# Kernel optimization log

Hardware: AMD Instinct MI355X
Metric: run time of the kernel (lower is better)

The kernel has to match this reference:

```python
import jax, jax.numpy as jnp
import numpy as np

IMG = 128; P = 16; ND = IMG // P; N = ND * ND  # 64 patches
INF = 3 * P * P      # 768 flattened patch features
ATT = 768; HID = 3072; OUT = 768; B = 64
EPS = 1e-5


def setup_inputs() -> dict:
    key = jax.random.key(0)
    ks = jax.random.split(key, 24)
    w = lambda k, shape: jax.random.normal(k, shape, jnp.float32) * 0.02
    return {
        "x": jax.random.normal(ks[0], (B, 3, IMG, IMG), jnp.float32),
        # per-patch q/k/v projections: [n, in, out] weights, [n, out] biases
        "Wq": w(ks[1], (N, INF, ATT)), "bq": w(ks[2], (N, ATT)),
        "Wk": w(ks[3], (N, INF, ATT)), "bk": w(ks[4], (N, ATT)),
        "Wv": w(ks[5], (N, INF, ATT)), "bv": w(ks[6], (N, ATT)),
        "ln_g": jnp.ones((ATT,), jnp.float32), "ln_b": jnp.zeros((ATT,), jnp.float32),
        "p1_w": w(ks[7], (INF, ATT)), "p1_b": w(ks[8], (ATT,)),
        "w0": w(ks[9], (ATT, HID)),  "b0": w(ks[10], (HID,)),
        "w1": w(ks[11], (HID, HID)), "b1": w(ks[12], (HID,)),
        "w2": w(ks[13], (HID, HID)), "b2": w(ks[14], (HID,)),
        "w3": w(ks[15], (HID, HID)), "b3": w(ks[16], (HID,)),
        "w4": w(ks[17], (HID, OUT)), "b4": w(ks[18], (OUT,)),
        "p2_w": w(ks[19], (ATT, OUT)), "p2_b": w(ks[20], (OUT,)),
    }


def _forward(x, Wq, bq, Wk, bk, Wv, bv, ln_g, ln_b, p1_w, p1_b,
             w0, b0, w1, b1, w2, b2, w3, b3, w4, b4, p2_w, p2_b):
    b_ = x.shape[0]
    # patch split (row-major over (i,j) blocks) then flatten channel*patch dims
    flat = x.reshape(b_, 3, ND, P, ND, P).transpose(0, 2, 4, 1, 3, 5).reshape(b_, N, INF)
    # per-patch projections, attention taken ACROSS the batch dim (as in source)
    q = jnp.einsum('bnf,nfd->bnd', flat, Wq) + bq
    k = jnp.einsum('bnf,nfd->bnd', flat, Wk) + bk
    v = jnp.einsum('bnf,nfd->bnd', flat, Wv) + bv
    scores = jnp.einsum('bnd,cnd->nbc', q, k) / jnp.sqrt(jnp.float32(ATT))  # [n,B,B]
    attn = jnp.einsum('nbc,cnd->bnd', jax.nn.softmax(scores, axis=-1), v)  # [B,n,ATT]
    # LayerNorm(att_features)
    mu = attn.mean(-1, keepdims=True)
    var = ((attn - mu) ** 2).mean(-1, keepdims=True)
    ln = (attn - mu) / jnp.sqrt(var + EPS) * ln_g + ln_b
    att = ln + flat @ p1_w + p1_b
    # linear stack (no nonlinearity in the source)
    h = att @ w0 + b0
    h = h @ w1 + b1
    h = h @ w2 + b2
    h = h @ w3 + b3
    h = h @ w4 + b4
    proj = h + att @ p2_w + p2_b
    return jax.nn.softmax(proj, axis=2)


def reference(x, Wq, bq, Wk, bk, Wv, bv, ln_g, ln_b, p1_w, p1_b,
              w0, b0, w1, b1, w2, b2, w3, b3, w4, b4, p2_w, p2_b):
    return _forward(x, Wq, bq, Wk, bk, Wv, bv, ln_g, ln_b, p1_w, p1_b,
                    w0, b0, w1, b1, w2, b2, w3, b3, w4, b4, p2_w, p2_b)
```

## Files before the change

### kernel.cpp

```cpp
#include <hip/hip_runtime.h>
#include <hip/hip_bf16.h>

using bf16 = __bf16;
using bf16x8 = __bf16 __attribute__((ext_vector_type(8)));
using f32x4 = float __attribute__((ext_vector_type(4)));

static constexpr long ROWEL = 64L * 768;

__device__ __forceinline__ void async16(void* lds, const void* g)
{
    __builtin_amdgcn_global_load_lds((const __attribute__((address_space(1))) void*)g,
                                     (__attribute__((address_space(3))) void*)lds, 16, 0, 0);
}

__global__ __launch_bounds__(256) void k_patchify(const float* __restrict__ x, bf16* __restrict__ flat)
{
    const int n = blockIdx.x;
    const int b = blockIdx.y;
    const int i_ = n >> 3, j_ = n & 7;
    for (int it = 0; it < 3; ++it) {
        int f = threadIdx.x + it * 256;
        int c = f >> 8, rem = f & 255, pi = rem >> 4, pj = rem & 15;
        float v = x[(((long)(b * 3 + c)) << 14) + ((i_ * 16 + pi) << 7) + (j_ * 16 + pj)];
        flat[(long)b * ROWEL + n * 768 + f] = (bf16)v;
    }
}

__global__ __launch_bounds__(256) void k_cvt_t2(
    const float* __restrict__ W0, bf16* __restrict__ T0,
    const float* __restrict__ W1, bf16* __restrict__ T1)
{
    const int z = blockIdx.z;
    const float* W = z ? W1 : W0;
    bf16* Wt = z ? T1 : T0;
    const int Kd = z ? 768 : 3072, Nd = 768;
    if (z && blockIdx.x >= 12) return;
    __shared__ bf16 T[64 * 66];
    const int k0 = blockIdx.x * 64, n0 = blockIdx.y * 64;
    const int tid = threadIdx.x;
    const int kr = tid >> 4, nc = (tid & 15) * 4;
#pragma unroll
    for (int i = 0; i < 4; ++i) {
        f32x4 v = *(const f32x4*)(W + (long)(k0 + kr + i * 16) * Nd + n0 + nc);
#pragma unroll
        for (int e = 0; e < 4; ++e)
            T[(kr + i * 16) * 66 + nc + e] = (bf16)v[e];
    }
    __syncthreads();
    const int nr = tid >> 3, ks = (tid & 7) * 8;
#pragma unroll
    for (int it = 0; it < 2; ++it) {
        int n = nr + it * 32;
        bf16x8 o;
#pragma unroll
        for (int j = 0; j < 8; ++j) o[j] = T[(ks + j) * 66 + n];
        *(bf16x8*)(Wt + (long)(n0 + n) * Kd + k0 + ks) = o;
    }
}

__global__ __launch_bounds__(256) void k_cast4(
    const float* __restrict__ s0, bf16* __restrict__ d0,
    const float* __restrict__ s1, bf16* __restrict__ d1,
    const float* __restrict__ s2, bf16* __restrict__ d2,
    const float* __restrict__ s3, bf16* __restrict__ d3)
{
    const int z = blockIdx.y;
    const float* W = z == 0 ? s0 : z == 1 ? s1 : z == 2 ? s2 : s3;
    bf16* o = z == 0 ? d0 : z == 1 ? d1 : z == 2 ? d2 : d3;
    const long nelem = z == 0 ? 768L * 3072 : 3072L * 3072;
    long i = ((long)blockIdx.x * 256 + threadIdx.x) * 8;
    if (i >= nelem) return;
    f32x4 a = *(const f32x4*)(W + i);
    f32x4 b = *(const f32x4*)(W + i + 4);
    bf16x8 v;
#pragma unroll
    for (int e = 0; e < 4; ++e) { v[e] = (bf16)a[e]; v[4 + e] = (bf16)b[e]; }
    *(bf16x8*)(o + i) = v;
}

template<int BM, int BN>
__global__ __launch_bounds__(256) void k_gemm_bt(
    const bf16* __restrict__ A, long lda,
    const bf16* __restrict__ Bt, long ldb,
    int K,
    const float* __restrict__ bias,
    const float* __restrict__ addm,
    const float* __restrict__ addt, long atld,
    bf16* __restrict__ Cb, float* __restrict__ Cf, long ldc)
{
    constexpr int WM = BM / 2, WN = BN / 2, FM = WM / 16, FN = WN / 16;
    __shared__ bf16 As[2][BM * 32];
    __shared__ bf16 Bs[2][BN * 32];
    const int tid = threadIdx.x, lane = tid & 63, wave = tid >> 6;
    const int wm = wave >> 1, wn = wave & 1;
    const long m0 = (long)blockIdx.x * BM, n0 = (long)blockIdx.y * BN;

    f32x4 acc[FM][FN];
#pragma unroll
    for (int i = 0; i < FM; ++i)
#pragma unroll
        for (int j = 0; j < FN; ++j) acc[i][j] = (f32x4){0.f, 0.f, 0.f, 0.f};

    const int nk = K >> 5;

    auto stage = [&](int buf, int kt) {
        const long kb = (long)kt * 32;
#pragma unroll
        for (int i = 0; i < BM / 64; ++i) {
            const int c = i * 256 + tid;
            const int r = c >> 2, seg = c & 3;
            async16(&As[buf][(i * 256 + wave * 64) * 8], A + (m0 + r) * lda + kb + seg * 8);
        }
#pragma unroll
        for (int i = 0; i < BN / 64; ++i) {
            const int c = i * 256 + tid;
            const int r = c >> 2, seg = c & 3;
            async16(&Bs[buf][(i * 256 + wave * 64) * 8], Bt + (n0 + r) * ldb + kb + seg * 8);
        }
    };

    stage(0, 0);
    __syncthreads();
    int cur = 0;
    for (int kt = 0; kt < nk; ++kt) {
        if (kt + 1 < nk) stage(cur ^ 1, kt + 1);
        bf16x8 af[FM], bfr[FN];
#pragma unroll
        for (int i = 0; i < FM; ++i)
            af[i] = *(const bf16x8*)&As[cur][(wm * WM + i * 16 + (lane & 15)) * 32 + (lane >> 4) * 8];
#pragma unroll
        for (int j = 0; j < FN; ++j)
            bfr[j] = *(const bf16x8*)&Bs[cur][(wn * WN + j * 16 + (lane & 15)) * 32 + (lane >> 4) * 8];
#pragma unroll
        for (int i = 0; i < FM; ++i)
#pragma unroll
            for (int j = 0; j < FN; ++j)
                acc[i][j] = __builtin_amdgcn_mfma_f32_16x16x32_bf16(af[i], bfr[j], acc[i][j], 0, 0, 0);
        __syncthreads();
        cur ^= 1;
    }

#pragma unroll
    for (int j = 0; j < FN; ++j) {
        const long col = n0 + wn * WN + j * 16 + (lane & 15);
        const float bb = bias ? bias[col] : 0.f;
#pragma unroll
        for (int i = 0; i < FM; ++i) {
#pragma unroll
            for (int r = 0; r < 4; ++r) {
                const long row = m0 + wm * WM + i * 16 + (lane >> 4) * 4 + r;
                const long idx = row * ldc + col;
                float v = acc[i][j][r] + bb;
                if (addm) v += addm[idx];
                if (addt) v += addt[col * atld + row];
                if (Cb) Cb[idx] = (bf16)v;
                if (Cf) Cf[idx] = v;
            }
        }
    }
}

__global__ __launch_bounds__(256) void k_qkv(
    const bf16* __restrict__ flat,
    const float* __restrict__ Wq, const float* __restrict__ Wk, const float* __restrict__ Wv,
    const float* __restrict__ bq, const float* __restrict__ bk, const float* __restrict__ bv,
    bf16* __restrict__ qo, bf16* __restrict__ ko, bf16* __restrict__ vo)
{
    const int zz = blockIdx.z;
    const float* W = zz == 0 ? Wq : zz == 1 ? Wk : Wv;
    const float* bias = zz == 0 ? bq : zz == 1 ? bk : bv;
    bf16* out = zz == 0 ? qo : zz == 1 ? ko : vo;

    __shared__ bf16 As[2][64 * 32];
    __shared__ float Bs[2][32 * 64];
    const int tid = threadIdx.x, lane = tid & 63, wave = tid >> 6;
    const int wm = wave >> 1, wn = wave & 1;
    const int n0 = blockIdx.x * 64;
    const int z = blockIdx.y;
    const float* Wz = W + (long)z * 589824;

    f32x4 acc[2][2];
#pragma unroll
    for (int i = 0; i < 2; ++i)
#pragma unroll
        for (int j = 0; j < 2; ++j) acc[i][j] = (f32x4){0.f, 0.f, 0.f, 0.f};

    auto stage = [&](int buf, int kt) {
        const int kb = kt * 32;
        {
            const int r = tid >> 2, seg = tid & 3;
            async16(&As[buf][wave * 512], flat + (long)r * ROWEL + z * 768 + kb + seg * 8);
        }
#pragma unroll
        for (int i = 0; i < 2; ++i) {
            const int c = i * 256 + tid;
            const int kl = c >> 4, nn = (c & 15) * 4;
            async16(&Bs[buf][(i * 256 + wave * 64) * 4], Wz + (long)(kb + kl) * 768 + n0 + nn);
        }
    };

    stage(0, 0);
    __syncthreads();
    int cur = 0;
    for (int kt = 0; kt < 24; ++kt) {
        if (kt + 1 < 24) stage(cur ^ 1, kt + 1);
        bf16x8 af[2], bfr[2];
#pragma unroll
        for (int i = 0; i < 2; ++i)
            af[i] = *(const bf16x8*)&As[cur][(wm * 32 + i * 16 + (lane & 15)) * 32 + (lane >> 4) * 8];
#pragma unroll
        for (int j = 0; j < 2; ++j) {
            const int n = wn * 32 + j * 16 + (lane & 15);
            const int kf = (lane >> 4) * 8;
            bf16x8 b;
#pragma unroll
            for (int e = 0; e < 8; ++e) b[e] = (bf16)Bs[cur][(kf + e) * 64 + n];
            bfr[j] = b;
        }
#pragma unroll
        for (int i = 0; i < 2; ++i)
#pragma unroll
            for (int j = 0; j < 2; ++j)
                acc[i][j] = __builtin_amdgcn_mfma_f32_16x16x32_bf16(af[i], bfr[j], acc[i][j], 0, 0, 0);
        __syncthreads();
        cur ^= 1;
    }

#pragma unroll
    for (int j = 0; j < 2; ++j) {
        const int col = n0 + wn * 32 + j * 16 + (lane & 15);
        const float bb = bias[z * 768 + col];
#pragma unroll
        for (int i = 0; i < 2; ++i) {
#pragma unroll
            for (int r = 0; r < 4; ++r) {
                const int row = wm * 32 + i * 16 + (lane >> 4) * 4 + r;
                out[(long)row * ROWEL + z * 768 + col] = (bf16)(acc[i][j][r] + bb);
            }
        }
    }
}

template<typename TW>
__global__ __launch_bounds__(256) void k_vm2(
    const float* __restrict__ Pin, const float* __restrict__ bin, const TW* __restrict__ W,
    int K, int N, float* __restrict__ Pout)
{
    __shared__ float red[4][64];
    const int tid = threadIdx.x;
    const int nl = tid & 63, kq = tid >> 6;
    const int n = blockIdx.x * 64 + nl;
    const int kc = blockIdx.y;
    const int kchunk = K / 8, kslice = kchunk / 4;
    const int k0 = kc * kchunk + kq * kslice;
    float acc = 0.f;
#pragma unroll 4
    for (int k = k0; k < k0 + kslice; ++k) {
        float vk = bin[k];
        if (Pin) {
#pragma unroll
            for (int j = 0; j < 8; ++j) vk += Pin[(long)j * K + k];
        }
        acc += vk * (float)W[(long)k * N + n];
    }
    red[kq][nl] = acc;
    __syncthreads();
    if (kq == 0)
        Pout[(long)kc * N + n] = red[0][nl] + red[1][nl] + red[2][nl] + red[3][nl];
}

__global__ __launch_bounds__(256) void k_vred(
    const float* __restrict__ P, const float* __restrict__ b1, const float* __restrict__ b2,
    int N, float* __restrict__ out)
{
    const int n = blockIdx.x * 256 + threadIdx.x;
    if (n >= N) return;
    float s = b1[n] + (b2 ? b2[n] : 0.f);
#pragma unroll
    for (int j = 0; j < 8; ++j) s += P[(long)j * N + n];
    out[n] = s;
}

__global__ __launch_bounds__(256) void k_attn(
    const bf16* __restrict__ q, const bf16* __restrict__ k, const bf16* __restrict__ v,
    float* __restrict__ attn)
{
    const int n = blockIdx.x;
    __shared__ bf16 QT[64 * 72];
    __shared__ bf16 KT[64 * 72];
    __shared__ float S[64 * 66];
    __shared__ bf16 P[64 * 72];
    __shared__ bf16 VT[128 * 72];

    const int tid = threadIdx.x, lane = tid & 63, wave = tid >> 6;
    const int wm = wave >> 1, wn = wave & 1;

    f32x4 accs[2][2];
#pragma unroll
    for (int i = 0; i < 2; ++i)
#pragma unroll
        for (int j = 0; j < 2; ++j) accs[i][j] = (f32x4){0.f, 0.f, 0.f, 0.f};

    for (int kt = 0; kt < 12; ++kt) {
#pragma unroll
        for (int i = 0; i < 2; ++i) {
            int cid = tid + i * 256;
            int r = cid >> 3, seg = cid & 7;
            *(bf16x8*)&QT[r * 72 + seg * 8] = *(const bf16x8*)(q + (long)r * ROWEL + n * 768 + kt * 64 + seg * 8);
            *(bf16x8*)&KT[r * 72 + seg * 8] = *(const bf16x8*)(k + (long)r * ROWEL + n * 768 + kt * 64 + seg * 8);
        }
        __syncthreads();
#pragma unroll
        for (int ks = 0; ks < 2; ++ks) {
            bf16x8 qa[2], kb[2];
#pragma unroll
            for (int i = 0; i < 2; ++i)
                qa[i] = *(const bf16x8*)&QT[(wm * 32 + i * 16 + (lane & 15)) * 72 + ks * 32 + (lane >> 4) * 8];
#pragma unroll
            for (int j = 0; j < 2; ++j)
                kb[j] = *(const bf16x8*)&KT[(wn * 32 + j * 16 + (lane & 15)) * 72 + ks * 32 + (lane >> 4) * 8];
#pragma unroll
            for (int i = 0; i < 2; ++i)
#pragma unroll
                for (int j = 0; j < 2; ++j)
                    accs[i][j] = __builtin_amdgcn_mfma_f32_16x16x32_bf16(qa[i], kb[j], accs[i][j], 0, 0, 0);
        }
        __syncthreads();
    }
    const float sc = 0.03608439182435161f;
#pragma unroll
    for (int i = 0; i < 2; ++i)
#pragma unroll
        for (int j = 0; j < 2; ++j)
#pragma unroll
            for (int r = 0; r < 4; ++r)
                S[(wm * 32 + i * 16 + (lane >> 4) * 4 + r) * 66 + wn * 32 + j * 16 + (lane & 15)] = accs[i][j][r] * sc;
    __syncthreads();

    {
        int r = tid >> 2, l4 = tid & 3;
        float m = -1e30f;
        for (int c = l4; c < 64; c += 4) m = fmaxf(m, S[r * 66 + c]);
        m = fmaxf(m, __shfl_xor(m, 1));
        m = fmaxf(m, __shfl_xor(m, 2));
        float s = 0.f;
        for (int c = l4; c < 64; c += 4) { float e = __expf(S[r * 66 + c] - m); S[r * 66 + c] = e; s += e; }
        s += __shfl_xor(s, 1);
        s += __shfl_xor(s, 2);
        float inv = 1.f / s;
        for (int c = l4; c < 64; c += 4) P[r * 72 + c] = (bf16)(S[r * 66 + c] * inv);
    }
    __syncthreads();

    for (int dc = 0; dc < 6; ++dc) {
#pragma unroll
        for (int i = 0; i < 4; ++i) {
            int cid = tid + i * 256;
            int c = cid >> 4, seg = cid & 15;
            bf16x8 vv = *(const bf16x8*)(v + (long)c * ROWEL + n * 768 + dc * 128 + seg * 8);
#pragma unroll
            for (int e = 0; e < 8; ++e)
                VT[(seg * 8 + e) * 72 + c] = vv[e];
        }
        __syncthreads();
        f32x4 acco[2][4];
#pragma unroll
        for (int i = 0; i < 2; ++i)
#pragma unroll
            for (int j = 0; j < 4; ++j) acco[i][j] = (f32x4){0.f, 0.f, 0.f, 0.f};
#pragma unroll
        for (int ks = 0; ks < 2; ++ks) {
            bf16x8 pa[2], vb[4];
#pragma unroll
            for (int i = 0; i < 2; ++i)
                pa[i] = *(const bf16x8*)&P[(wm * 32 + i * 16 + (lane & 15)) * 72 + ks * 32 + (lane >> 4) * 8];
#pragma unroll
            for (int j = 0; j < 4; ++j)
                vb[j] = *(const bf16x8*)&VT[(wn * 64 + j * 16 + (lane & 15)) * 72 + ks * 32 + (lane >> 4) * 8];
#pragma unroll
            for (int i = 0; i < 2; ++i)
#pragma unroll
                for (int j = 0; j < 4; ++j)
                    acco[i][j] = __builtin_amdgcn_mfma_f32_16x16x32_bf16(pa[i], vb[j], acco[i][j], 0, 0, 0);
        }
#pragma unroll
        for (int i = 0; i < 2; ++i)
#pragma unroll
            for (int j = 0; j < 4; ++j)
#pragma unroll
                for (int r = 0; r < 4; ++r) {
                    long b = wm * 32 + i * 16 + (lane >> 4) * 4 + r;
                    int d = dc * 128 + wn * 64 + j * 16 + (lane & 15);
                    attn[b * ROWEL + n * 768 + d] = acco[i][j][r];
                }
        __syncthreads();
    }
}

__global__ __launch_bounds__(256) void k_ln(float* __restrict__ a,
                                            const float* __restrict__ g, const float* __restrict__ bb)
{
    const long row = blockIdx.x * 4 + (threadIdx.x >> 6);
    const int lane = threadIdx.x & 63;
    float* p = a + row * 768;
    f32x4 xv[3];
    float s = 0.f;
#pragma unroll
    for (int c = 0; c < 3; ++c) {
        xv[c] = *(const f32x4*)(p + c * 256 + lane * 4);
        s += xv[c][0] + xv[c][1] + xv[c][2] + xv[c][3];
    }
#pragma unroll
    for (int o = 1; o < 64; o <<= 1) s += __shfl_xor(s, o);
    const float mu = s * (1.f / 768.f);
    float vs = 0.f;
#pragma unroll
    for (int c = 0; c < 3; ++c)
#pragma unroll
        for (int e = 0; e < 4; ++e) { float d = xv[c][e] - mu; vs += d * d; }
#pragma unroll
    for (int o = 1; o < 64; o <<= 1) vs += __shfl_xor(vs, o);
    const float rstd = rsqrtf(vs * (1.f / 768.f) + 1e-5f);
#pragma unroll
    for (int c = 0; c < 3; ++c)
#pragma unroll
        for (int e = 0; e < 4; ++e) {
            int col = c * 256 + lane * 4 + e;
            p[col] = (xv[c][e] - mu) * rstd * g[col] + bb[col];
        }
}

__global__ __launch_bounds__(256) void k_softmax(float* __restrict__ o)
{
    const long row = blockIdx.x * 4 + (threadIdx.x >> 6);
    const int lane = threadIdx.x & 63;
    float* p = o + row * 768;
    f32x4 xv[3];
    float m = -1e30f;
#pragma unroll
    for (int c = 0; c < 3; ++c) {
        xv[c] = *(const f32x4*)(p + c * 256 + lane * 4);
        m = fmaxf(m, fmaxf(fmaxf(xv[c][0], xv[c][1]), fmaxf(xv[c][2], xv[c][3])));
    }
#pragma unroll
    for (int o2 = 1; o2 < 64; o2 <<= 1) m = fmaxf(m, __shfl_xor(m, o2));
    float s = 0.f;
#pragma unroll
    for (int c = 0; c < 3; ++c)
#pragma unroll
        for (int e = 0; e < 4; ++e) { float ev = __expf(xv[c][e] - m); xv[c][e] = ev; s += ev; }
#pragma unroll
    for (int o2 = 1; o2 < 64; o2 <<= 1) s += __shfl_xor(s, o2);
    const float inv = 1.f / s;
#pragma unroll
    for (int c = 0; c < 3; ++c)
        *(f32x4*)(p + c * 256 + lane * 4) = xv[c] * inv;
}

extern "C" void kernel_launch(void* const* d_in, const int* in_sizes, int n_in,
                              void* d_out, int out_size, void* d_ws, size_t ws_size,
                              hipStream_t stream)
{
    const float* x   = (const float*)d_in[0];
    const float* Wq  = (const float*)d_in[1];
    const float* bq  = (const float*)d_in[2];
    const float* Wk  = (const float*)d_in[3];
    const float* bk  = (const float*)d_in[4];
    const float* Wv  = (const float*)d_in[5];
    const float* bv  = (const float*)d_in[6];
    const float* lng = (const float*)d_in[7];
    const float* lnb = (const float*)d_in[8];
    const float* p1w = (const float*)d_in[9];
    const float* p1b = (const float*)d_in[10];
    const float* w0  = (const float*)d_in[11];
    const float* b0  = (const float*)d_in[12];
    const float* w1  = (const float*)d_in[13];
    const float* b1  = (const float*)d_in[14];
    const float* w2  = (const float*)d_in[15];
    const float* b2  = (const float*)d_in[16];
    const float* w3  = (const float*)d_in[17];
    const float* b3  = (const float*)d_in[18];
    const float* w4  = (const float*)d_in[19];
    const float* b4  = (const float*)d_in[20];
    const float* p2w = (const float*)d_in[21];
    const float* p2b = (const float*)d_in[22];
    float* out = (float*)d_out;

    char* wsbase = (char*)d_ws;
    size_t off = 0;
    auto alloc = [&](size_t bytes) { char* p = wsbase + off; off += (bytes + 255) & ~(size_t)255; return p; };
    bf16*  flat = (bf16*)alloc(4096L * 768 * 2);
    bf16*  qb   = (bf16*)alloc(4096L * 768 * 2);
    bf16*  kb   = (bf16*)alloc(4096L * 768 * 2);
    bf16*  vb2  = (bf16*)alloc(4096L * 768 * 2);
    float* attn = (float*)alloc(4096L * 768 * 4);
    bf16*  att  = (bf16*)alloc(4096L * 768 * 2);
    bf16*  p1t  = (bf16*)alloc(768L * 768 * 2);
    bf16*  w4t  = (bf16*)alloc(768L * 3072 * 2);
    bf16*  w0c  = (bf16*)alloc(768L * 3072 * 2);
    bf16*  w1c  = (bf16*)alloc(3072L * 3072 * 2);
    bf16*  w2c  = (bf16*)alloc(3072L * 3072 * 2);
    bf16*  w3c  = (bf16*)alloc(3072L * 3072 * 2);
    bf16*  M1   = (bf16*)alloc(768L * 3072 * 2);
    bf16*  M2   = (bf16*)alloc(768L * 3072 * 2);
    bf16*  M3   = (bf16*)alloc(768L * 3072 * 2);
    bf16*  Mt   = (bf16*)alloc(768L * 768 * 2);
    float* vPa  = (float*)alloc(8L * 3072 * 4);
    float* vPb  = (float*)alloc(8L * 3072 * 4);
    float* c4   = (float*)alloc(768 * 4);
    if (off > ws_size) return;

    k_patchify<<<dim3(64, 64), 256, 0, stream>>>(x, flat);
    k_cast4<<<dim3(4608, 4), 256, 0, stream>>>(w0, w0c, w1, w1c, w2, w2c, w3, w3c);
    k_cvt_t2<<<dim3(48, 12, 2), 256, 0, stream>>>(w4, w4t, p1w, p1t);

    k_qkv<<<dim3(12, 64, 3), 256, 0, stream>>>(flat, Wq, Wk, Wv, bq, bk, bv, qb, kb, vb2);

    k_attn<<<64, 256, 0, stream>>>(qb, kb, vb2, attn);
    k_ln<<<1024, 256, 0, stream>>>(attn, lng, lnb);
    k_gemm_bt<64, 128><<<dim3(64, 6), 256, 0, stream>>>(flat, 768, p1t, 768, 768, p1b, attn, nullptr, 0, att, nullptr, 768);

    k_gemm_bt<64, 64><<<dim3(12, 48), 256, 0, stream>>>(w4t, 3072, w3c, 3072, 3072, nullptr, nullptr, nullptr, 0, M1, nullptr, 3072);
    k_gemm_bt<64, 64><<<dim3(12, 48), 256, 0, stream>>>(M1, 3072, w2c, 3072, 3072, nullptr, nullptr, nullptr, 0, M2, nullptr, 3072);
    k_gemm_bt<64, 64><<<dim3(12, 48), 256, 0, stream>>>(M2, 3072, w1c, 3072, 3072, nullptr, nullptr, nullptr, 0, M3, nullptr, 3072);
    k_gemm_bt<64, 64><<<dim3(12, 12), 256, 0, stream>>>(M3, 3072, w0c, 3072, 3072, nullptr, nullptr, p2w, 768, Mt, nullptr, 768);

    k_vm2<bf16><<<dim3(48, 8), 256, 0, stream>>>(nullptr, b0, w1c, 3072, 3072, vPa);
    k_vm2<bf16><<<dim3(48, 8), 256, 0, stream>>>(vPa, b1, w2c, 3072, 3072, vPb);
    k_vm2<bf16><<<dim3(48, 8), 256, 0, stream>>>(vPb, b2, w3c, 3072, 3072, vPa);
    k_vm2<float><<<dim3(12, 8), 256, 0, stream>>>(vPa, b3, w4, 3072, 768, vPb);
    k_vred<<<3, 256, 0, stream>>>(vPb, b4, p2b, 768, c4);

    k_gemm_bt<64, 128><<<dim3(64, 6), 256, 0, stream>>>(att, 768, Mt, 768, 768, c4, nullptr, nullptr, 0, nullptr, out, 768);
    k_softmax<<<1024, 256, 0, stream>>>(out);
}
```

Measured before the change: 606.5 us.

## Split-K the weight-chain GEMMs and use smaller tiles for activation GEMMs

```diff
diff --git a/kernel.cpp b/kernel.cpp
--- a/kernel.cpp
+++ b/kernel.cpp
@@ -2,6 +2,7 @@
 #include <hip/hip_bf16.h>
 
 using bf16 = __bf16;
+using bf16x4 = __bf16 __attribute__((ext_vector_type(4)));
 using bf16x8 = __bf16 __attribute__((ext_vector_type(8)));
 using f32x4 = float __attribute__((ext_vector_type(4)));
 
@@ -85,7 +86,6 @@
     int K,
     const float* __restrict__ bias,
     const float* __restrict__ addm,
-    const float* __restrict__ addt, long atld,
     bf16* __restrict__ Cb, float* __restrict__ Cf, long ldc)
 {
     constexpr int WM = BM / 2, WN = BN / 2, FM = WM / 16, FN = WN / 16;
@@ -152,11 +152,112 @@
                 const long idx = row * ldc + col;
                 float v = acc[i][j][r] + bb;
                 if (addm) v += addm[idx];
-                if (addt) v += addt[col * atld + row];
                 if (Cb) Cb[idx] = (bf16)v;
                 if (Cf) Cf[idx] = v;
             }
         }
+    }
+}
+
+template<int BM, int BN>
+__global__ __launch_bounds__(256) void k_gemm_btsk(
+    const bf16* __restrict__ A, long lda,
+    const bf16* __restrict__ Bt, long ldb,
+    int Ks,
+    float* __restrict__ Cp, long zstride, long ldc)
+{
+    constexpr int WM = BM / 2, WN = BN / 2, FM = WM / 16, FN = WN / 16;
+    __shared__ bf16 As[2][BM * 32];
+    __shared__ bf16 Bs[2][BN * 32];
+    const int tid = threadIdx.x, lane = tid & 63, wave = tid >> 6;
+    const int wm = wave >> 1, wn = wave & 1;
+    const long m0 = (long)blockIdx.x * BM, n0 = (long)blockIdx.y * BN;
+    const long kofs = (long)blockIdx.z * Ks;
+
+    f32x4 acc[FM][FN];
+#pragma unroll
+    for (int i = 0; i < FM; ++i)
+#pragma unroll
+        for (int j = 0; j < FN; ++j) acc[i][j] = (f32x4){0.f, 0.f, 0.f, 0.f};
+
+    const int nk = Ks >> 5;
+
+    auto stage = [&](int buf, int kt) {
+        const long kb = kofs + (long)kt * 32;
+#pragma unroll
+        for (int i = 0; i < BM / 64; ++i) {
+            const int c = i * 256 + tid;
+            const int r = c >> 2, seg = c & 3;
+            async16(&As[buf][(i * 256 + wave * 64) * 8], A + (m0 + r) * lda + kb + seg * 8);
+        }
+#pragma unroll
+        for (int i = 0; i < BN / 64; ++i) {
+            const int c = i * 256 + tid;
+            const int r = c >> 2, seg = c & 3;
+            async16(&Bs[buf][(i * 256 + wave * 64) * 8], Bt + (n0 + r) * ldb + kb + seg * 8);
+        }
+    };
+
+    stage(0, 0);
+    __syncthreads();
+    int cur = 0;
+    for (int kt = 0; kt < nk; ++kt) {
+        if (kt + 1 < nk) stage(cur ^ 1, kt + 1);
+        bf16x8 af[FM], bfr[FN];
+#pragma unroll
+        for (int i = 0; i < FM; ++i)
+            af[i] = *(const bf16x8*)&As[cur][(wm * WM + i * 16 + (lane & 15)) * 32 + (lane >> 4) * 8];
+#pragma unroll
+        for (int j = 0; j < FN; ++j)
+            bfr[j] = *(const bf16x8*)&Bs[cur][(wn * WN + j * 16 + (lane & 15)) * 32 + (lane >> 4) * 8];
+#pragma unroll
+        for (int i = 0; i < FM; ++i)
+#pragma unroll
+            for (int j = 0; j < FN; ++j)
+                acc[i][j] = __builtin_amdgcn_mfma_f32_16x16x32_bf16(af[i], bfr[j], acc[i][j], 0, 0, 0);
+        __syncthreads();
+        cur ^= 1;
+    }
+
+    float* Cz = Cp + (long)blockIdx.z * zstride;
+#pragma unroll
+    for (int j = 0; j < FN; ++j) {
+        const long col = n0 + wn * WN + j * 16 + (lane & 15);
+#pragma unroll
+        for (int i = 0; i < FM; ++i)
+#pragma unroll
+            for (int r = 0; r < 4; ++r) {
+                const long row = m0 + wm * WM + i * 16 + (lane >> 4) * 4 + r;
+                Cz[row * ldc + col] = acc[i][j][r];
+            }
+    }
+}
+
+__global__ __launch_bounds__(256) void k_skadd(
+    const float* __restrict__ P, long zstride, int S, long nelem, bf16* __restrict__ out)
+{
+    long i = ((long)blockIdx.x * 256 + threadIdx.x) * 4;
+    if (i >= nelem) return;
+    f32x4 s = *(const f32x4*)(P + i);
+    for (int z = 1; z < S; ++z) {
+        f32x4 p = *(const f32x4*)(P + (long)z * zstride + i);
+        s += p;
+    }
+    bf16x4 o;
+#pragma unroll
+    for (int e = 0; e < 4; ++e) o[e] = (bf16)s[e];
+    *(bf16x4*)(out + i) = o;
+}
+
+__global__ __launch_bounds__(256) void k_skaddT(
+    const float* __restrict__ P, long zstride, int S,
+    const float* __restrict__ p2w, bf16* __restrict__ Mt)
+{
+    const int n = blockIdx.x;
+    for (int k = threadIdx.x; k < 768; k += 256) {
+        float s = p2w[(long)k * 768 + n];
+        for (int z = 0; z < S; ++z) s += P[(long)z * zstride + n * 768 + k];
+        Mt[n * 768 + k] = (bf16)s;
     }
 }
 
@@ -505,11 +606,15 @@
     bf16*  M2   = (bf16*)alloc(768L * 3072 * 2);
     bf16*  M3   = (bf16*)alloc(768L * 3072 * 2);
     bf16*  Mt   = (bf16*)alloc(768L * 768 * 2);
+    float* Cp   = (float*)alloc(3L * 768 * 3072 * 4);
     float* vPa  = (float*)alloc(8L * 3072 * 4);
     float* vPb  = (float*)alloc(8L * 3072 * 4);
     float* c4   = (float*)alloc(768 * 4);
     if (off > ws_size) return;
 
+    const long ZS = 768L * 3072;
+    const long ZS4 = 768L * 768;
+
     k_patchify<<<dim3(64, 64), 256, 0, stream>>>(x, flat);
     k_cast4<<<dim3(4608, 4), 256, 0, stream>>>(w0, w0c, w1, w1c, w2, w2c, w3, w3c);
     k_cvt_t2<<<dim3(48, 12, 2), 256, 0, stream>>>(w4, w4t, p1w, p1t);
@@ -518,12 +623,16 @@
 
     k_attn<<<64, 256, 0, stream>>>(qb, kb, vb2, attn);
     k_ln<<<1024, 256, 0, stream>>>(attn, lng, lnb);
-    k_gemm_bt<64, 128><<<dim3(64, 6), 256, 0, stream>>>(flat, 768, p1t, 768, 768, p1b, attn, nullptr, 0, att, nullptr, 768);
-
-    k_gemm_bt<64, 64><<<dim3(12, 48), 256, 0, stream>>>(w4t, 3072, w3c, 3072, 3072, nullptr, nullptr, nullptr, 0, M1, nullptr, 3072);
-    k_gemm_bt<64, 64><<<dim3(12, 48), 256, 0, stream>>>(M1, 3072, w2c, 3072, 3072, nullptr, nullptr, nullptr, 0, M2, nullptr, 3072);
-    k_gemm_bt<64, 64><<<dim3(12, 48), 256, 0, stream>>>(M2, 3072, w1c, 3072, 3072, nullptr, nullptr, nullptr, 0, M3, nullptr, 3072);
-    k_gemm_bt<64, 64><<<dim3(12, 12), 256, 0, stream>>>(M3, 3072, w0c, 3072, 3072, nullptr, nullptr, p2w, 768, Mt, nullptr, 768);
+    k_gemm_bt<64, 64><<<dim3(64, 12), 256, 0, stream>>>(flat, 768, p1t, 768, 768, p1b, attn, att, nullptr, 768);
+
+    k_gemm_btsk<64, 64><<<dim3(12, 48, 3), 256, 0, stream>>>(w4t, 3072, w3c, 3072, 1024, Cp, ZS, 3072);
+    k_skadd<<<2304, 256, 0, stream>>>(Cp, ZS, 3, ZS, M1);
+    k_gemm_btsk<64, 64><<<dim3(12, 48, 3), 256, 0, stream>>>(M1, 3072, w2c, 3072, 1024, Cp, ZS, 3072);
+    k_skadd<<<2304, 256, 0, stream>>>(Cp, ZS, 3, ZS, M2);
+    k_gemm_btsk<64, 64><<<dim3(12, 48, 3), 256, 0, stream>>>(M2, 3072, w1c, 3072, 1024, Cp, ZS, 3072);
+    k_skadd<<<2304, 256, 0, stream>>>(Cp, ZS, 3, ZS, M3);
+    k_gemm_btsk<64, 64><<<dim3(12, 12, 6), 256, 0, stream>>>(M3, 3072, w0c, 3072, 512, Cp, ZS4, 768);
+    k_skaddT<<<768, 256, 0, stream>>>(Cp, ZS4, 6, p2w, Mt);
 
     k_vm2<bf16><<<dim3(48, 8), 256, 0, stream>>>(nullptr, b0, w1c, 3072, 3072, vPa);
     k_vm2<bf16><<<dim3(48, 8), 256, 0, stream>>>(vPa, b1, w2c, 3072, 3072, vPb);
@@ -531,6 +640,6 @@
     k_vm2<float><<<dim3(12, 8), 256, 0, stream>>>(vPa, b3, w4, 3072, 768, vPb);
     k_vred<<<3, 256, 0, stream>>>(vPb, b4, p2b, 768, c4);
 
-    k_gemm_bt<64, 128><<<dim3(64, 6), 256, 0, stream>>>(att, 768, Mt, 768, 768, c4, nullptr, nullptr, 0, nullptr, out, 768);
+    k_gemm_bt<64, 64><<<dim3(64, 12), 256, 0, stream>>>(att, 768, Mt, 768, 768, c4, nullptr, nullptr, out, 768);
     k_softmax<<<1024, 256, 0, stream>>>(out);
 }
```

New measurement: 570.1 us. -6.0%, faster.
